# Kernel tuning notes

Measured on AMD Instinct MI355X. Metric: run time of the kernel, lower is better.

The kernel has to match this reference:

```python
import jax, jax.numpy as jnp
import numpy as np

NEG_INF = -1e20

# Dims: s=512 samples, b=2048 background, t=32 trees, f=64 features, h=128 hidden, y=1
S, B, T, F, H, Y = 512, 2048, 32, 64, 128, 1


def setup_inputs() -> dict:
    key = jax.random.key(0)
    ks = jax.random.split(key, 8)
    X = jax.random.normal(ks[0], (S, F), dtype=jnp.float32)
    background_X = jax.random.normal(ks[1], (B, F), dtype=jnp.float32)
    background_y = jax.random.normal(ks[2], (B, Y), dtype=jnp.float32)
    neighbors_hot = jax.random.randint(ks[3], (S, B, T), 0, 2).astype(jnp.bool_)
    # encoder params: Linear(F->H), Tanh, Linear(H->H)  (n_layers=2)
    W1 = jax.random.normal(ks[4], (F, H), dtype=jnp.float32) / np.sqrt(F)
    b1 = jnp.zeros((H,), dtype=jnp.float32)
    W2 = jax.random.normal(ks[5], (H, H), dtype=jnp.float32) / np.sqrt(H)
    b2 = jnp.zeros((H,), dtype=jnp.float32)
    return {"X": X, "background_X": background_X, "background_y": background_y,
            "neighbors_hot": neighbors_hot, "W1": W1, "b1": b1, "W2": W2, "b2": b2}


def reference(X, background_X, background_y, neighbors_hot, W1, b1, W2, b2):
    def encode(x):
        return jnp.tanh(x @ W1 + b1) @ W2 + b2  # Linear-Tanh-Linear

    X_enc = encode(X)                    # (s, h)
    bg_enc = encode(background_X)        # (b, h)
    dots = X_enc @ bg_enc.T              # (s, b)
    # broadcast over trees + mask, softmax over background axis
    scores = jnp.where(neighbors_hot, dots[:, :, None], NEG_INF)  # (s, b, t)
    first_alphas = jax.nn.softmax(scores, axis=1)                 # (s, b, t)
    first_leaf_xs = jnp.einsum('sbt,bf->stf', first_alphas, background_X)
    first_leaf_y = jnp.einsum('sbt,by->sty', first_alphas, background_y)
    return first_leaf_xs, first_leaf_y, first_alphas
```

## Files before the change

### kernel.cpp

```cpp
#include <hip/hip_runtime.h>
#include <hip/hip_bf16.h>

#define NS 512
#define NB 2048
#define NT 32
#define NF 64
#define NH 128
#define NFX 80

#define OY  ((size_t)NS * NT * NF)
#define OA  (OY + (size_t)NS * NT)

#define PACK_B 2048
#define ENC_B  1280
#define TR_B   32

typedef __attribute__((ext_vector_type(8))) short bf16x8;
typedef __attribute__((ext_vector_type(4))) float f32x4;

__device__ __forceinline__ unsigned short f2bfu(float x) {
    __hip_bfloat16 h = __float2bfloat16(x);
    return __builtin_bit_cast(unsigned short, h);
}

__device__ __forceinline__ unsigned int pack16_bytes(uint4 v) {
    unsigned int r = 0;
    unsigned int xs[4] = {v.x, v.y, v.z, v.w};
    #pragma unroll
    for (int i = 0; i < 4; ++i) {
        unsigned int x = xs[i];
        unsigned int t = (x | ((x & 0x7F7F7F7Fu) + 0x7F7F7F7Fu)) & 0x80808080u;
        t >>= 7;
        unsigned int n = (t | (t >> 7) | (t >> 14) | (t >> 21)) & 0xFu;
        r |= n << (i * 4);
    }
    return r;
}

__global__ __launch_bounds__(256) void prep_k(const void* mask,
        unsigned long long* pm,
        const float* __restrict__ X, const float* __restrict__ bgX,
        const float* __restrict__ bgy,
        const float* __restrict__ W1, const float* __restrict__ b1,
        const float* __restrict__ W2, const float* __restrict__ b2,
        float* __restrict__ enc, unsigned short* __restrict__ bgXT2) {
    __shared__ float cbuf[64 * 65];
    const int blk = blockIdx.x;
    const int tid = threadIdx.x;

    if (blk < PACK_B) {
        int* flagp = (int*)cbuf;
        if (tid == 0) *flagp = 0;
        __syncthreads();
        {
            uint4 v = ((const uint4*)mask)[tid];
            if (((v.x | v.y | v.z | v.w) & 0xFFFFFF00u) != 0u) *flagp = 1;
        }
        __syncthreads();
        const int isbyte = *flagp;

        const int w = blk * 256 + tid;
        if (isbyte) {
            const uint4* mb = (const uint4*)mask;
            uint4 q0 = mb[(size_t)w * 4 + 0];
            uint4 q1 = mb[(size_t)w * 4 + 1];
            uint4 q2 = mb[(size_t)w * 4 + 2];
            uint4 q3 = mb[(size_t)w * 4 + 3];
            unsigned long long r =  (unsigned long long)pack16_bytes(q0)
                                 | ((unsigned long long)pack16_bytes(q1) << 16)
                                 | ((unsigned long long)pack16_bytes(q2) << 32)
                                 | ((unsigned long long)pack16_bytes(q3) << 48);
            pm[w] = r;
        } else {
            const uint4* mi = (const uint4*)mask;
            unsigned long long r = 0;
            #pragma unroll
            for (int i = 0; i < 16; ++i) {
                uint4 v = mi[(size_t)w * 16 + i];
                unsigned int b = (v.x ? 1u : 0u) | (v.y ? 2u : 0u) |
                                 (v.z ? 4u : 0u) | (v.w ? 8u : 0u);
                r |= (unsigned long long)b << (i * 4);
            }
            pm[w] = r;
        }
        return;
    }

    if (blk < PACK_B + ENC_B) {
        const int r0 = (blk - PACK_B) * 2;
        float* xr = cbuf;
        float* hr = cbuf + 128;
        if (tid < 128) {
            int r = tid >> 6, c = tid & 63;
            int row = r0 + r;
            const float* src = (row < NS) ? (X + (size_t)row * NF)
                                          : (bgX + (size_t)(row - NS) * NF);
            xr[r * 64 + c] = src[c];
        }
        __syncthreads();
        const int j = tid & 127, h = tid >> 7;
        const float* xh = xr + h * 64;
        float a1 = b1[j];
        #pragma unroll 4
        for (int f = 0; f < NF; ++f)
            a1 = fmaf(xh[f], W1[f * NH + j], a1);
        hr[h * 128 + j] = tanhf(a1);
        __syncthreads();
        const float* hh = hr + h * 128;
        float a2 = b2[j];
        #pragma unroll 4
        for (int k = 0; k < NH; ++k)
            a2 = fmaf(hh[k], W2[k * NH + j], a2);
        enc[(size_t)(r0 + h) * NH + j] = a2;
        return;
    }

    {
        const int b0 = (blk - PACK_B - ENC_B) * 64;
        float (*t_lds)[65] = (float(*)[65])cbuf;
        #pragma unroll
        for (int it = 0; it < 4; ++it) {
            int idx = (it * 256 + tid) * 4;
            int r = idx >> 6, c = idx & 63;
            *(float4*)(&t_lds[r][c]) = *(const float4*)(bgX + (size_t)(b0 + r) * NF + c);
        }
        __syncthreads();
        const int f = tid >> 2, sg = (tid & 3) * 16;
        union { unsigned short u[16]; uint4 q[2]; } pk;
        #pragma unroll
        for (int i = 0; i < 16; ++i) pk.u[i] = f2bfu(t_lds[sg + i][f]);
        uint4* dst = (uint4*)(bgXT2 + (size_t)f * NB + b0 + sg);
        dst[0] = pk.q[0];
        dst[1] = pk.q[1];
        if (tid < 64) {
            int b = b0 + tid;
            bgXT2[(size_t)64 * NB + b] = f2bfu(bgy[b]);
            bgXT2[(size_t)65 * NB + b] = 0x3F80;
            #pragma unroll
            for (int ff = 66; ff < NFX; ++ff) bgXT2[(size_t)ff * NB + b] = 0;
        }
    }
}

__global__ __launch_bounds__(256) void dots_k(const float* __restrict__ Xe,
        const float* __restrict__ Be, float* __restrict__ dots) {
    __shared__ float At[64 * 68];
    __shared__ float Bt[64 * 68];
    const int s0 = blockIdx.y * 64, b0 = blockIdx.x * 64;
    const int tid = threadIdx.x;
    const int ts = tid & 15, tb = tid >> 4;
    float acc[4][4] = {};
    for (int kt = 0; kt < 2; ++kt) {
        __syncthreads();
        #pragma unroll
        for (int it = 0; it < 4; ++it) {
            int idx = tid * 4 + it * 1024;
            int r = idx >> 6, k = idx & 63;
            *(float4*)(&At[r * 68 + k]) = *(const float4*)(Xe + (size_t)(s0 + r) * NH + kt * 64 + k);
            *(float4*)(&Bt[r * 68 + k]) = *(const float4*)(Be + (size_t)(b0 + r) * NH + kt * 64 + k);
        }
        __syncthreads();
        #pragma unroll 4
        for (int k = 0; k < 64; ++k) {
            float a[4], bv[4];
            #pragma unroll
            for (int i = 0; i < 4; ++i) a[i] = At[(ts + 16 * i) * 68 + k];
            #pragma unroll
            for (int jj = 0; jj < 4; ++jj) bv[jj] = Bt[(tb * 4 + jj) * 68 + k];
            #pragma unroll
            for (int i = 0; i < 4; ++i)
                #pragma unroll
                for (int jj = 0; jj < 4; ++jj)
                    acc[i][jj] = fmaf(a[i], bv[jj], acc[i][jj]);
        }
    }
    #pragma unroll
    for (int i = 0; i < 4; ++i) {
        float4 v = make_float4(acc[i][0], acc[i][1], acc[i][2], acc[i][3]);
        *(float4*)(&dots[(size_t)(s0 + ts + 16 * i) * NB + b0 + tb * 4]) = v;
    }
}

__global__ __launch_bounds__(256) void fusedA_k(float* __restrict__ dots,
        const unsigned long long* __restrict__ pmask,
        const unsigned short* __restrict__ bgXT2,
        float* __restrict__ rden_g, float* __restrict__ out) {
    __shared__ __align__(16) unsigned int mrow[NB];
    __shared__ __align__(16) unsigned short e_bf[NB];
    __shared__ float part[3 * NT * NFX];
    __shared__ float wmax[4];
    __shared__ float rden_l[NT];
    __shared__ float ytmp[NT];

    const int s = blockIdx.x;
    const int tid = threadIdx.x;
    const int lane = tid & 63, w = tid >> 6;
    const int lo = lane & 15, hi = lane >> 4;

    float* drow = dots + (size_t)s * NB;
    float4 d0 = *(const float4*)(drow + tid * 8);
    float4 d1 = *(const float4*)(drow + tid * 8 + 4);
    const uint4* pmrow = (const uint4*)((const unsigned int*)pmask + (size_t)s * NB);
    *(uint4*)(&mrow[tid * 4]) = pmrow[tid];
    *(uint4*)(&mrow[(tid + 256) * 4]) = pmrow[tid + 256];
    float pmax = fmaxf(fmaxf(fmaxf(d0.x, d0.y), fmaxf(d0.z, d0.w)),
                       fmaxf(fmaxf(d1.x, d1.y), fmaxf(d1.z, d1.w)));
    #pragma unroll
    for (int off = 32; off >= 1; off >>= 1)
        pmax = fmaxf(pmax, __shfl_xor(pmax, off, 64));
    if (lane == 0) wmax[w] = pmax;
    __syncthreads();
    const float Ms = fmaxf(fmaxf(wmax[0], wmax[1]), fmaxf(wmax[2], wmax[3]));
    float ev[8] = {d0.x, d0.y, d0.z, d0.w, d1.x, d1.y, d1.z, d1.w};
    union { unsigned short u[8]; uint4 q; } epk;
    #pragma unroll
    for (int q = 0; q < 8; ++q) { ev[q] = __expf(ev[q] - Ms); epk.u[q] = f2bfu(ev[q]); }
    *(float4*)(drow + tid * 8)     = make_float4(ev[0], ev[1], ev[2], ev[3]);
    *(float4*)(drow + tid * 8 + 4) = make_float4(ev[4], ev[5], ev[6], ev[7]);
    *(uint4*)(&e_bf[tid * 8]) = epk.q;
    __syncthreads();

    f32x4 acc[2][5] = {};
    const unsigned short* bptr = bgXT2 + (size_t)lo * NB + w * 512 + hi * 8;
    #pragma unroll 2
    for (int ks = 0; ks < 16; ++ks) {
        const int bb = w * 512 + ks * 32 + hi * 8;
        uint4 ew4 = *(const uint4*)(&e_bf[bb]);
        uint4 m0 = *(const uint4*)(&mrow[bb]);
        uint4 m1 = *(const uint4*)(&mrow[bb + 4]);
        unsigned int ew[4] = {ew4.x, ew4.y, ew4.z, ew4.w};
        unsigned int mv[8] = {m0.x, m0.y, m0.z, m0.w, m1.x, m1.y, m1.z, m1.w};
        unsigned int A0[4], A1[4];
        #pragma unroll
        for (int p = 0; p < 4; ++p) {
            unsigned int mlo = mv[2 * p]     >> lo;
            unsigned int mhi = mv[2 * p + 1] >> lo;
            unsigned int k0 = ((mlo & 1u)       ? 0x0000FFFFu : 0u) |
                              ((mhi & 1u)       ? 0xFFFF0000u : 0u);
            unsigned int k1 = ((mlo & 0x10000u) ? 0x0000FFFFu : 0u) |
                              ((mhi & 0x10000u) ? 0xFFFF0000u : 0u);
            A0[p] = ew[p] & k0;
            A1[p] = ew[p] & k1;
        }
        bf16x8 a0 = __builtin_bit_cast(bf16x8, make_uint4(A0[0], A0[1], A0[2], A0[3]));
        bf16x8 a1 = __builtin_bit_cast(bf16x8, make_uint4(A1[0], A1[1], A1[2], A1[3]));
        #pragma unroll
        for (int n = 0; n < 5; ++n) {
            uint4 bv = *(const uint4*)(bptr + (size_t)n * 16 * NB + ks * 32);
            bf16x8 bfr = __builtin_bit_cast(bf16x8, bv);
            acc[0][n] = __builtin_amdgcn_mfma_f32_16x16x32_bf16(a0, bfr, acc[0][n], 0, 0, 0);
            acc[1][n] = __builtin_amdgcn_mfma_f32_16x16x32_bf16(a1, bfr, acc[1][n], 0, 0, 0);
        }
    }

    if (w > 0) {
        #pragma unroll
        for (int m = 0; m < 2; ++m)
            #pragma unroll
            for (int n = 0; n < 5; ++n)
                #pragma unroll
                for (int r = 0; r < 4; ++r) {
                    int t = m * 16 + hi * 4 + r, f = n * 16 + lo;
                    part[(w - 1) * (NT * NFX) + t * NFX + f] = acc[m][n][r];
                }
    }
    __syncthreads();
    if (w == 0) {
        #pragma unroll
        for (int m = 0; m < 2; ++m)
            #pragma unroll
            for (int r = 0; r < 4; ++r) {
                int t = m * 16 + hi * 4 + r;
                int o = t * NFX + 64 + lo;
                float tot = acc[m][4][r] + part[o] + part[NT * NFX + o] + part[2 * NT * NFX + o];
                if (lo == 0) ytmp[t] = tot;
                if (lo == 1) rden_l[t] = (tot > 0.f) ? 1.f / tot : 0.f;
            }
    }
    __syncthreads();
    if (w == 0) {
        float* xout = out + (size_t)s * NT * NF;
        #pragma unroll
        for (int m = 0; m < 2; ++m)
            #pragma unroll
            for (int n = 0; n < 4; ++n)
                #pragma unroll
                for (int r = 0; r < 4; ++r) {
                    int t = m * 16 + hi * 4 + r, f = n * 16 + lo;
                    int o = t * NFX + f;
                    float tot = acc[m][n][r] + part[o] + part[NT * NFX + o] + part[2 * NT * NFX + o];
                    xout[t * NF + f] = tot * rden_l[t];
                }
    }
    if (tid < 32) {
        out[OY + (size_t)s * NT + tid] = ytmp[tid] * rden_l[tid];
        rden_g[(size_t)s * NT + tid] = rden_l[tid];
    }
}

__global__ __launch_bounds__(256) void alphas_k(const float* __restrict__ e,
        const unsigned int* __restrict__ pmask32, const float* __restrict__ rden_g,
        float* __restrict__ out) {
    const int tid = threadIdx.x;
    const int blk = blockIdx.x;
    const int s = blk >> 3;
    const int tq = tid & 7;
    const f32x4 rd4 = *(const f32x4*)(rden_g + (size_t)s * NT + tq * 4);
    const float* erow = e + (size_t)s * NB;
    const unsigned int* mr = pmask32 + (size_t)s * NB;
    float* aout = out + OA + (size_t)s * NB * NT;
    const int b0 = (blk & 7) * 256 + (tid >> 3);

    float ev[8];
    unsigned int mv[8];
    #pragma unroll
    for (int j = 0; j < 8; ++j) {
        ev[j] = erow[b0 + j * 32];
        mv[j] = mr[b0 + j * 32] >> (tq * 4);
    }
    #pragma unroll
    for (int j = 0; j < 8; ++j) {
        const int b = b0 + j * 32;
        f32x4 v;
        v.x = (mv[j] & 1u) ? ev[j] * rd4.x : 0.f;
        v.y = (mv[j] & 2u) ? ev[j] * rd4.y : 0.f;
        v.z = (mv[j] & 4u) ? ev[j] * rd4.z : 0.f;
        v.w = (mv[j] & 8u) ? ev[j] * rd4.w : 0.f;
        *(f32x4*)(aout + (size_t)b * NT + tq * 4) = v;
    }
}

extern "C" void kernel_launch(void* const* d_in, const int* in_sizes, int n_in,
                              void* d_out, int out_size, void* d_ws, size_t ws_size,
                              hipStream_t stream) {
    (void)in_sizes; (void)n_in; (void)out_size; (void)ws_size;
    const float* X   = (const float*)d_in[0];
    const float* bgX = (const float*)d_in[1];
    const float* bgy = (const float*)d_in[2];
    const void*  nh  = d_in[3];
    const float* W1  = (const float*)d_in[4];
    const float* b1v = (const float*)d_in[5];
    const float* W2  = (const float*)d_in[6];
    const float* b2v = (const float*)d_in[7];
    float* out = (float*)d_out;
    char* ws = (char*)d_ws;

    float* enc = (float*)(ws + 4096);
    float* rden_g = (float*)(ws + 4096);
    float* Xe = enc;
    float* Be = enc + (size_t)NS * NH;
    float* dots = (float*)(ws + 4096 + (size_t)(NS + NB) * NH * 4);
    unsigned long long* pmask = (unsigned long long*)((char*)dots + (size_t)NS * NB * 4);
    unsigned short* bgXT2 = (unsigned short*)((char*)pmask + (size_t)NS * NB * NT / 64 * 8);

    prep_k<<<PACK_B + ENC_B + TR_B, 256, 0, stream>>>(nh, pmask, X, bgX, bgy,
                                                      W1, b1v, W2, b2v, enc, bgXT2);
    dots_k<<<dim3(NB / 64, NS / 64), 256, 0, stream>>>(Xe, Be, dots);
    fusedA_k<<<NS, 256, 0, stream>>>(dots, pmask, bgXT2, rden_g, out);
    alphas_k<<<NS * 8, 256, 0, stream>>>(dots, (const unsigned int*)pmask, rden_g, out);
}
```

Measured before the change: 105.4 us.

## Coalesce mask packing, pre-swizzle bgX into MFMA fragment order, transpose B tile

Mask packing now has each wave read contiguous 16-byte chunks across lanes and combine them with lane shuffles, so global reads are coalesced instead of strided per thread. The transposed background features are written in a layout that matches the MFMA B-fragment order, so the fused kernel loads each fragment as one contiguous 64-lane uint4 read instead of loads strided by NB. The dots kernel stores the B tile transposed in LDS so each thread reads one float4 per k instead of four scalars. The cost is more complex indexing, scalar transposed LDS stores that may bank-conflict, and a producer and consumer that must agree on the new layout.

New measurement: 98.32 us. 6.7% less time.

```diff
diff --git a/kernel.cpp b/kernel.cpp
--- a/kernel.cpp
+++ b/kernel.cpp
@@ -44,7 +44,7 @@
         const float* __restrict__ W1, const float* __restrict__ b1,
         const float* __restrict__ W2, const float* __restrict__ b2,
         float* __restrict__ enc, unsigned short* __restrict__ bgXT2) {
-    __shared__ float cbuf[64 * 65];
+    __shared__ float cbuf[64 * 68];
     const int blk = blockIdx.x;
     const int tid = threadIdx.x;
 
@@ -59,29 +59,36 @@
         __syncthreads();
         const int isbyte = *flagp;
 
-        const int w = blk * 256 + tid;
+        const int wv = tid >> 6, lane = tid & 63;
+        unsigned long long* pmw = pm + (size_t)blk * 256 + wv * 64;
         if (isbyte) {
-            const uint4* mb = (const uint4*)mask;
-            uint4 q0 = mb[(size_t)w * 4 + 0];
-            uint4 q1 = mb[(size_t)w * 4 + 1];
-            uint4 q2 = mb[(size_t)w * 4 + 2];
-            uint4 q3 = mb[(size_t)w * 4 + 3];
-            unsigned long long r =  (unsigned long long)pack16_bytes(q0)
-                                 | ((unsigned long long)pack16_bytes(q1) << 16)
-                                 | ((unsigned long long)pack16_bytes(q2) << 32)
-                                 | ((unsigned long long)pack16_bytes(q3) << 48);
-            pm[w] = r;
+            const char* base = (const char*)mask + (size_t)blk * 16384 + wv * 4096;
+            #pragma unroll
+            for (int k = 0; k < 4; ++k) {
+                uint4 q = *(const uint4*)(base + k * 1024 + lane * 16);
+                unsigned int p = pack16_bytes(q);
+                unsigned int p1 = (unsigned int)__shfl_down((int)p, 1, 64);
+                unsigned int r32 = p | (p1 << 16);
+                unsigned int h32 = (unsigned int)__shfl_down((int)r32, 2, 64);
+                if ((lane & 3) == 0)
+                    pmw[k * 16 + (lane >> 2)] =
+                        (unsigned long long)r32 | ((unsigned long long)h32 << 32);
+            }
         } else {
-            const uint4* mi = (const uint4*)mask;
-            unsigned long long r = 0;
-            #pragma unroll
-            for (int i = 0; i < 16; ++i) {
-                uint4 v = mi[(size_t)w * 16 + i];
-                unsigned int b = (v.x ? 1u : 0u) | (v.y ? 2u : 0u) |
+            const char* base = (const char*)mask + (size_t)blk * 65536 + wv * 16384;
+            #pragma unroll 4
+            for (int k = 0; k < 16; ++k) {
+                uint4 v = *(const uint4*)(base + k * 1024 + lane * 16);
+                unsigned int r = (v.x ? 1u : 0u) | (v.y ? 2u : 0u) |
                                  (v.z ? 4u : 0u) | (v.w ? 8u : 0u);
-                r |= (unsigned long long)b << (i * 4);
-            }
-            pm[w] = r;
+                r |= ((unsigned int)__shfl_down((int)r, 1, 64)) << 4;
+                r |= ((unsigned int)__shfl_down((int)r, 2, 64)) << 8;
+                r |= ((unsigned int)__shfl_down((int)r, 4, 64)) << 16;
+                unsigned long long r64 = (unsigned long long)r |
+                    ((unsigned long long)(unsigned int)__shfl_down((int)r, 8, 64) << 32);
+                if ((lane & 15) == 0)
+                    pmw[k * 4 + (lane >> 4)] = r64;
+            }
         }
         return;
     }
@@ -116,7 +123,8 @@
     }
 
     {
-        const int b0 = (blk - PACK_B - ENC_B) * 64;
+        const int bb0 = blk - PACK_B - ENC_B;
+        const int b0 = bb0 * 64;
         float (*t_lds)[65] = (float(*)[65])cbuf;
         #pragma unroll
         for (int it = 0; it < 4; ++it) {
@@ -125,19 +133,26 @@
             *(float4*)(&t_lds[r][c]) = *(const float4*)(bgX + (size_t)(b0 + r) * NF + c);
         }
         __syncthreads();
-        const int f = tid >> 2, sg = (tid & 3) * 16;
-        union { unsigned short u[16]; uint4 q[2]; } pk;
-        #pragma unroll
-        for (int i = 0; i < 16; ++i) pk.u[i] = f2bfu(t_lds[sg + i][f]);
-        uint4* dst = (uint4*)(bgXT2 + (size_t)f * NB + b0 + sg);
-        dst[0] = pk.q[0];
-        dst[1] = pk.q[1];
-        if (tid < 64) {
-            int b = b0 + tid;
-            bgXT2[(size_t)64 * NB + b] = f2bfu(bgy[b]);
-            bgXT2[(size_t)65 * NB + b] = 0x3F80;
-            #pragma unroll
-            for (int ff = 66; ff < NFX; ++ff) bgXT2[(size_t)ff * NB + b] = 0;
+        uint4* fb = (uint4*)bgXT2;
+        const int c2 = tid >> 7;
+        const int cg = bb0 * 2 + c2;
+        for (int idx = tid & 127; idx < 320; idx += 128) {
+            const int n = idx >> 6, l = idx & 63;
+            const int lo = l & 15, hi = l >> 4;
+            union { unsigned short u[8]; uint4 q; } pk;
+            if (n < 4) {
+                #pragma unroll
+                for (int j = 0; j < 8; ++j)
+                    pk.u[j] = f2bfu(t_lds[c2 * 32 + hi * 8 + j][n * 16 + lo]);
+            } else {
+                #pragma unroll
+                for (int j = 0; j < 8; ++j) {
+                    if (lo == 0)      pk.u[j] = f2bfu(bgy[b0 + c2 * 32 + hi * 8 + j]);
+                    else if (lo == 1) pk.u[j] = 0x3F80;
+                    else              pk.u[j] = 0;
+                }
+            }
+            fb[((size_t)cg * 5 + n) * 64 + l] = pk.q;
         }
     }
 }
@@ -148,7 +163,7 @@
     __shared__ float Bt[64 * 68];
     const int s0 = blockIdx.y * 64, b0 = blockIdx.x * 64;
     const int tid = threadIdx.x;
-    const int ts = tid & 15, tb = tid >> 4;
+    const int ts = tid >> 4, tb = tid & 15;
     float acc[4][4] = {};
     for (int kt = 0; kt < 2; ++kt) {
         __syncthreads();
@@ -157,21 +172,26 @@
             int idx = tid * 4 + it * 1024;
             int r = idx >> 6, k = idx & 63;
             *(float4*)(&At[r * 68 + k]) = *(const float4*)(Xe + (size_t)(s0 + r) * NH + kt * 64 + k);
-            *(float4*)(&Bt[r * 68 + k]) = *(const float4*)(Be + (size_t)(b0 + r) * NH + kt * 64 + k);
+            float4 bvv = *(const float4*)(Be + (size_t)(b0 + r) * NH + kt * 64 + k);
+            Bt[(k + 0) * 68 + r] = bvv.x;
+            Bt[(k + 1) * 68 + r] = bvv.y;
+            Bt[(k + 2) * 68 + r] = bvv.z;
+            Bt[(k + 3) * 68 + r] = bvv.w;
         }
         __syncthreads();
         #pragma unroll 4
         for (int k = 0; k < 64; ++k) {
-            float a[4], bv[4];
+            float4 bq = *(const float4*)(&Bt[k * 68 + tb * 4]);
+            float a[4];
             #pragma unroll
             for (int i = 0; i < 4; ++i) a[i] = At[(ts + 16 * i) * 68 + k];
             #pragma unroll
-            for (int jj = 0; jj < 4; ++jj) bv[jj] = Bt[(tb * 4 + jj) * 68 + k];
-            #pragma unroll
-            for (int i = 0; i < 4; ++i)
-                #pragma unroll
-                for (int jj = 0; jj < 4; ++jj)
-                    acc[i][jj] = fmaf(a[i], bv[jj], acc[i][jj]);
+            for (int i = 0; i < 4; ++i) {
+                acc[i][0] = fmaf(a[i], bq.x, acc[i][0]);
+                acc[i][1] = fmaf(a[i], bq.y, acc[i][1]);
+                acc[i][2] = fmaf(a[i], bq.z, acc[i][2]);
+                acc[i][3] = fmaf(a[i], bq.w, acc[i][3]);
+            }
         }
     }
     #pragma unroll
@@ -221,7 +241,7 @@
     __syncthreads();
 
     f32x4 acc[2][5] = {};
-    const unsigned short* bptr = bgXT2 + (size_t)lo * NB + w * 512 + hi * 8;
+    const uint4* fb = (const uint4*)bgXT2;
     #pragma unroll 2
     for (int ks = 0; ks < 16; ++ks) {
         const int bb = w * 512 + ks * 32 + hi * 8;
@@ -244,9 +264,10 @@
         }
         bf16x8 a0 = __builtin_bit_cast(bf16x8, make_uint4(A0[0], A0[1], A0[2], A0[3]));
         bf16x8 a1 = __builtin_bit_cast(bf16x8, make_uint4(A1[0], A1[1], A1[2], A1[3]));
+        const uint4* fr = fb + ((size_t)(w * 16 + ks) * 5) * 64 + lane;
         #pragma unroll
         for (int n = 0; n < 5; ++n) {
-            uint4 bv = *(const uint4*)(bptr + (size_t)n * 16 * NB + ks * 32);
+            uint4 bv = fr[n * 64];
             bf16x8 bfr = __builtin_bit_cast(bf16x8, bv);
             acc[0][n] = __builtin_amdgcn_mfma_f32_16x16x32_bf16(a0, bfr, acc[0][n], 0, 0, 0);
             acc[1][n] = __builtin_amdgcn_mfma_f32_16x16x32_bf16(a1, bfr, acc[1][n], 0, 0, 0);
```
